# Optimization experiments

Hardware: AMD Instinct MI355X
Metric: run time of the kernel (lower is better)

Reference implementation:

```python
import jax, jax.numpy as jnp
import numpy as np

B, N, NC, DIM, H, D, M, TOPK = 1, 2048, 2048, 1024, 16, 64, 16, 64


def _l2norm(t):
    # F.normalize(t, p=2, dim=-1)
    return t / jnp.clip(jnp.linalg.norm(t, axis=-1, keepdims=True), 1e-12)


def _attn_layer(x, ctx, q_mask, k_mask, Wq, Wk, Wv, th_pre, th_post,
                mem_k, mem_v, scale_p, hs, Wo):
    b, n, _ = x.shape
    h, m, d = mem_k.shape
    nc = ctx.shape[1]
    q = (x @ Wq).reshape(b, n, h, d).transpose(0, 2, 1, 3)      # b h i d
    k = (ctx @ Wk).reshape(b, nc, h, d).transpose(0, 2, 1, 3)   # b h j d
    v = (ctx @ Wv).reshape(b, nc, h, d).transpose(0, 2, 1, 3)
    # memory key/values prepended
    k = jnp.concatenate([jnp.broadcast_to(mem_k[None], (b, h, m, d)), k], axis=2)
    v = jnp.concatenate([jnp.broadcast_to(mem_v[None], (b, h, m, d)), v], axis=2)
    # input mask (q_mask x k_mask), padded True over mem slots
    im = q_mask[:, None, :, None] & k_mask[:, None, None, :]    # b 1 i j
    im = jnp.pad(im, ((0, 0), (0, 0), (0, 0), (m, 0)), constant_values=True)
    # qk_norm: cosine-sim attention with learned per-head scale
    q = _l2norm(q)
    k = _l2norm(k)
    scale = 1.0 / jnp.clip(jnp.exp(scale_p), 0.01)              # [h]
    dots = jnp.einsum('bhid,bhjd->bhij', q, k) * scale[None, :, None, None]
    dots = jnp.einsum('gh,bhij->bgij', th_pre, dots)            # pre-softmax talking heads (1x1 conv over heads)
    neg = -jnp.finfo(dots.dtype).max
    dots = jnp.where(im, dots, neg)
    # sparse topk: keep only the TOPK largest logits per query
    kth = jax.lax.top_k(dots, TOPK)[0][..., -1:]
    dots = jnp.where(dots < kth, neg, dots)
    attn = jax.nn.softmax(dots, axis=-1)
    attn = jnp.einsum('gh,bhij->bgij', th_post, attn)           # post-softmax talking heads
    out = jnp.einsum('bhij,bhjd->bhid', attn, v)
    out = out * hs[None, :, None, None]                          # head scale
    out = out.transpose(0, 2, 1, 3).reshape(b, n, h * d)
    return out @ Wo


def setup_inputs():
    key = jax.random.key(0)
    ks = jax.random.split(key, 18)
    s = 1.0 / np.sqrt(DIM)
    sh = 1.0 / np.sqrt(H)

    def w(i, shape, scale=1.0):
        return jax.random.normal(ks[i], shape, dtype=jnp.float32) * scale

    return {
        'x': w(0, (B, N, DIM)),
        'context': w(1, (2, B, NC, DIM)),
        'mask': jnp.ones((B, N), dtype=bool),
        'context_mask': jnp.ones((B, NC), dtype=bool),
        'Wq1': w(2, (DIM, H * D), s), 'Wk1': w(3, (DIM, H * D), s), 'Wv1': w(4, (DIM, H * D), s),
        'Wq2': w(5, (DIM, H * D), s), 'Wk2': w(6, (DIM, H * D), s), 'Wv2': w(7, (DIM, H * D), s),
        'th_pre1': w(8, (H, H), sh), 'th_post1': w(9, (H, H), sh),
        'th_pre2': w(10, (H, H), sh), 'th_post2': w(11, (H, H), sh),
        'mem_k1': w(12, (H, M, D)), 'mem_v1': w(13, (H, M, D)),
        'mem_k2': w(14, (H, M, D)), 'mem_v2': w(15, (H, M, D)),
        'scale1': jnp.full((H,), -3.0, jnp.float32),
        'scale2': jnp.full((H,), -3.0, jnp.float32),
        'head_scale1': jnp.ones((H,), jnp.float32),
        'head_scale2': jnp.ones((H,), jnp.float32),
        'Wo1': w(16, (H * D, DIM), s), 'Wo2': w(17, (H * D, DIM), s),
    }


def reference(x, context, mask, context_mask,
              Wq1, Wk1, Wv1, Wq2, Wk2, Wv2,
              th_pre1, th_post1, th_pre2, th_post2,
              mem_k1, mem_v1, mem_k2, mem_v2,
              scale1, scale2, head_scale1, head_scale2, Wo1, Wo2):
    x = _attn_layer(x, context[0], mask, context_mask, Wq1, Wk1, Wv1,
                    th_pre1, th_post1, mem_k1, mem_v1, scale1, head_scale1, Wo1)
    x = _attn_layer(x, context[1], mask, context_mask, Wq2, Wk2, Wv2,
                    th_pre2, th_post2, mem_k2, mem_v2, scale2, head_scale2, Wo2)
    return x
```

## Files before the change

kernel.cpp:

```cpp
#include <hip/hip_runtime.h>

#define DEVI __device__ __forceinline__

typedef unsigned short u16;
typedef __attribute__((ext_vector_type(8))) _Float16 f16x8;
typedef __attribute__((ext_vector_type(4))) float f32x4;

#define NQ   2048
#define DIMM 1024
#define HD   16
#define MM   16
#define JTOT 2064
#define JPK  2080
#define JPAD 2112
#define KTOP 64
#define EPITCH 2114

DEVI u16 f2h(float x) {
    _Float16 h = (_Float16)x;
    u16 r; __builtin_memcpy(&r, &h, 2); return r;
}
DEVI void fsplit(float x, u16& hi, u16& lo) {
    _Float16 h = (_Float16)x;
    float r = x - (float)h;
    _Float16 l = (_Float16)r;
    __builtin_memcpy(&hi, &h, 2);
    __builtin_memcpy(&lo, &l, 2);
}

__global__ __launch_bounds__(256) void split1_kernel(
    const float* __restrict__ s, u16* __restrict__ hi, u16* __restrict__ lo, int n4)
{
    int gid = blockIdx.x * 256 + threadIdx.x;
    if (gid < n4) {
        float4 v = ((const float4*)s)[gid];
        ushort4 h, l;
        fsplit(v.x, h.x, l.x); fsplit(v.y, h.y, l.y);
        fsplit(v.z, h.z, l.z); fsplit(v.w, h.w, l.w);
        ((ushort4*)hi)[gid] = h;
        ((ushort4*)lo)[gid] = l;
    }
}

struct P8 { const float* w[8]; };

__global__ __launch_bounds__(256) void wtrans_kernel(P8 src, u16* WTh, u16* WTl) {
    __shared__ float T[64][65];
    const float* W = src.w[blockIdx.z];
    size_t off = (size_t)blockIdx.z * DIMM * DIMM;
    int n0 = blockIdx.x * 64, k0 = blockIdx.y * 64;
#pragma unroll
    for (int rep = 0; rep < 16; ++rep) {
        int idx = rep * 256 + threadIdx.x;
        int kk = idx >> 6, nn = idx & 63;
        T[kk][nn] = W[(size_t)(k0 + kk) * DIMM + n0 + nn];
    }
    __syncthreads();
#pragma unroll
    for (int rep = 0; rep < 16; ++rep) {
        int idx = rep * 256 + threadIdx.x;
        int nn = idx >> 6, kk = idx & 63;
        u16 h, l; fsplit(T[kk][nn], h, l);
        WTh[off + (size_t)(n0 + nn) * DIMM + k0 + kk] = h;
        WTl[off + (size_t)(n0 + nn) * DIMM + k0 + kk] = l;
    }
}

template<int OM>
__global__ __launch_bounds__(256) void gemm_nt(
    const u16* __restrict__ A, int lda, long sA,
    const u16* __restrict__ B, int ldb, long sB,
    void* __restrict__ Cv, int ldc, long sC, int K)
{
    __shared__ u16 As[64 * 40];
    __shared__ u16 Bs[64 * 40];
    const int tid = threadIdx.x;
    const int z = blockIdx.z;
    A += (size_t)z * sA; B += (size_t)z * sB;
    const int bm = blockIdx.x * 64, bn = blockIdx.y * 64;
    const int l = tid & 63, w = tid >> 6;
    const int wm = (w >> 1) * 32, wn = (w & 1) * 32;
    const int srow = tid >> 2, skcol = (tid & 3) * 8;
    const u16* Ag = A + (size_t)(bm + srow) * lda + skcol;
    const u16* Bg = B + (size_t)(bn + srow) * ldb + skcol;
    const int lr = l & 15, lk = (l >> 4) * 8;
    f32x4 acc[2][2] = {};
    for (int k0 = 0; k0 < K; k0 += 32) {
        uint4 av = *(const uint4*)(Ag + k0);
        uint4 bv = *(const uint4*)(Bg + k0);
        __syncthreads();
        *(uint4*)&As[srow * 40 + skcol] = av;
        *(uint4*)&Bs[srow * 40 + skcol] = bv;
        __syncthreads();
        f16x8 a0 = *(const f16x8*)&As[(wm + lr) * 40 + lk];
        f16x8 a1 = *(const f16x8*)&As[(wm + 16 + lr) * 40 + lk];
        f16x8 b0 = *(const f16x8*)&Bs[(wn + lr) * 40 + lk];
        f16x8 b1 = *(const f16x8*)&Bs[(wn + 16 + lr) * 40 + lk];
        acc[0][0] = __builtin_amdgcn_mfma_f32_16x16x32_f16(a0, b0, acc[0][0], 0, 0, 0);
        acc[0][1] = __builtin_amdgcn_mfma_f32_16x16x32_f16(a0, b1, acc[0][1], 0, 0, 0);
        acc[1][0] = __builtin_amdgcn_mfma_f32_16x16x32_f16(a1, b0, acc[1][0], 0, 0, 0);
        acc[1][1] = __builtin_amdgcn_mfma_f32_16x16x32_f16(a1, b1, acc[1][1], 0, 0, 0);
    }
    const int crow0 = bm + wm + (l >> 4) * 4;
    const int ccol0 = bn + wn + lr;
#pragma unroll
    for (int mi = 0; mi < 2; ++mi)
#pragma unroll
        for (int ni = 0; ni < 2; ++ni)
#pragma unroll
            for (int r = 0; r < 4; ++r) {
                int row = crow0 + mi * 16 + r;
                int col = ccol0 + ni * 16;
                if (OM == 0) {
                    float* C = (float*)Cv + (size_t)z * sC;
                    C[(size_t)row * ldc + col] = acc[mi][ni][r];
                } else {
                    u16* C = (u16*)Cv + (size_t)z * sC;
                    C[(size_t)row * ldc + col] = f2h(acc[mi][ni][r]);
                }
            }
}

__global__ __launch_bounds__(256) void gemm3_nt(
    const u16* __restrict__ Ah, const u16* __restrict__ Al, int lda,
    const u16* __restrict__ Bh, const u16* __restrict__ Bl, int ldb,
    float* __restrict__ C, int ldc, int K)
{
    __shared__ u16 Ash[64 * 40];
    __shared__ u16 Asl[64 * 40];
    __shared__ u16 Bsh[64 * 40];
    __shared__ u16 Bsl[64 * 40];
    const int tid = threadIdx.x;
    const int bm = blockIdx.x * 64, bn = blockIdx.y * 64;
    const int l = tid & 63, w = tid >> 6;
    const int wm = (w >> 1) * 32, wn = (w & 1) * 32;
    const int srow = tid >> 2, skcol = (tid & 3) * 8;
    const size_t aoff = (size_t)(bm + srow) * lda + skcol;
    const size_t boff = (size_t)(bn + srow) * ldb + skcol;
    const int lr = l & 15, lk = (l >> 4) * 8;
    f32x4 acc[2][2] = {};
    for (int k0 = 0; k0 < K; k0 += 32) {
        uint4 avh = *(const uint4*)(Ah + aoff + k0);
        uint4 avl = *(const uint4*)(Al + aoff + k0);
        uint4 bvh = *(const uint4*)(Bh + boff + k0);
        uint4 bvl = *(const uint4*)(Bl + boff + k0);
        __syncthreads();
        *(uint4*)&Ash[srow * 40 + skcol] = avh;
        *(uint4*)&Asl[srow * 40 + skcol] = avl;
        *(uint4*)&Bsh[srow * 40 + skcol] = bvh;
        *(uint4*)&Bsl[srow * 40 + skcol] = bvl;
        __syncthreads();
        f16x8 a0h = *(const f16x8*)&Ash[(wm + lr) * 40 + lk];
        f16x8 a1h = *(const f16x8*)&Ash[(wm + 16 + lr) * 40 + lk];
        f16x8 a0l = *(const f16x8*)&Asl[(wm + lr) * 40 + lk];
        f16x8 a1l = *(const f16x8*)&Asl[(wm + 16 + lr) * 40 + lk];
        f16x8 b0h = *(const f16x8*)&Bsh[(wn + lr) * 40 + lk];
        f16x8 b1h = *(const f16x8*)&Bsh[(wn + 16 + lr) * 40 + lk];
        f16x8 b0l = *(const f16x8*)&Bsl[(wn + lr) * 40 + lk];
        f16x8 b1l = *(const f16x8*)&Bsl[(wn + 16 + lr) * 40 + lk];
#define MF(acc_, a_, b_) acc_ = __builtin_amdgcn_mfma_f32_16x16x32_f16(a_, b_, acc_, 0, 0, 0)
        MF(acc[0][0], a0h, b0h); MF(acc[0][0], a0h, b0l); MF(acc[0][0], a0l, b0h);
        MF(acc[0][1], a0h, b1h); MF(acc[0][1], a0h, b1l); MF(acc[0][1], a0l, b1h);
        MF(acc[1][0], a1h, b0h); MF(acc[1][0], a1h, b0l); MF(acc[1][0], a1l, b0h);
        MF(acc[1][1], a1h, b1h); MF(acc[1][1], a1h, b1l); MF(acc[1][1], a1l, b1h);
#undef MF
    }
    const int crow0 = bm + wm + (l >> 4) * 4;
    const int ccol0 = bn + wn + lr;
#pragma unroll
    for (int mi = 0; mi < 2; ++mi)
#pragma unroll
        for (int ni = 0; ni < 2; ++ni)
#pragma unroll
            for (int r = 0; r < 4; ++r)
                C[(size_t)(crow0 + mi * 16 + r) * ldc + ccol0 + ni * 16] = acc[mi][ni][r];
}

__global__ __launch_bounds__(256) void normq_kernel(
    const float* __restrict__ Qf, const float* __restrict__ scp,
    u16* __restrict__ qnh, u16* __restrict__ qnl)
{
    int w = threadIdx.x >> 6, l = threadIdx.x & 63;
    int wid = blockIdx.x * 4 + w;
    int h = wid >> 11, i = wid & 2047;
    float x = Qf[(size_t)i * DIMM + h * 64 + l];
    float ss = x * x;
#pragma unroll
    for (int m = 32; m; m >>= 1) ss += __shfl_xor(ss, m);
    float inv = 1.0f / fmaxf(sqrtf(ss), 1e-12f);
    float sc = 1.0f / fmaxf(expf(scp[h]), 0.01f);
    u16 hh, ll; fsplit(x * inv * sc, hh, ll);
    size_t idx = ((size_t)h * NQ + i) * 64 + l;
    qnh[idx] = hh; qnl[idx] = ll;
}

__global__ __launch_bounds__(256) void buildkn_kernel(
    const float* __restrict__ Kf, const float* __restrict__ mem_k,
    u16* __restrict__ knh, u16* __restrict__ knl)
{
    int w = threadIdx.x >> 6, l = threadIdx.x & 63;
    int wid = blockIdx.x * 4 + w;
    int h = wid / JPK, j = wid - h * JPK;
    float x = (j < MM) ? mem_k[((size_t)h * MM + j) * 64 + l]
            : (j < JTOT) ? Kf[(size_t)(j - MM) * DIMM + h * 64 + l] : 0.0f;
    float ss = x * x;
#pragma unroll
    for (int m = 32; m; m >>= 1) ss += __shfl_xor(ss, m);
    float inv = 1.0f / fmaxf(sqrtf(ss), 1e-12f);
    u16 hh, ll; fsplit(x * inv, hh, ll);
    size_t idx = ((size_t)h * JPK + j) * 64 + l;
    knh[idx] = hh; knl[idx] = ll;
}

__global__ __launch_bounds__(256) void buildvvT_kernel(
    const float* __restrict__ Vf, const float* __restrict__ mem_v,
    const float* __restrict__ hsp, u16* __restrict__ vvT)
{
    __shared__ float T[64][65];
    int h = blockIdx.z, j0 = blockIdx.x * 64;
    float hs = hsp[h];
#pragma unroll
    for (int rep = 0; rep < 16; ++rep) {
        int idx = rep * 256 + threadIdx.x;
        int jl = idx >> 6, d = idx & 63;
        int j = j0 + jl;
        float x = (j < MM) ? mem_v[((size_t)h * MM + j) * 64 + d]
                : (j < JTOT) ? Vf[(size_t)(j - MM) * DIMM + h * 64 + d] : 0.0f;
        T[jl][d] = x * hs;
    }
    __syncthreads();
#pragma unroll
    for (int rep = 0; rep < 16; ++rep) {
        int idx = rep * 256 + threadIdx.x;
        int d = idx >> 6, jl = idx & 63;
        vvT[((size_t)h * 64 + d) * JPAD + j0 + jl] = f2h(T[jl][d]);
    }
}

__global__ __launch_bounds__(256) void dots_kernel(
    const u16* __restrict__ qnh, const u16* __restrict__ qnl,
    const u16* __restrict__ knh, const u16* __restrict__ knl,
    const float* __restrict__ th_pre, float* __restrict__ D,
    int q0, int NQC)
{
    __shared__ float red[4][8][256];
    const int tid = threadIdx.x, l = tid & 63, w = tid >> 6;
    const int it = blockIdx.x * 16;
    const int jt = blockIdx.y * 16;
    const int lr = l & 15, lk = (l >> 4) * 8;
    const int qrow = q0 + it + lr;
    const int jrow = jt + lr;
    f32x4 accg[16] = {};
#pragma unroll
    for (int hh = 0; hh < 4; ++hh) {
        const int h = w * 4 + hh;
        size_t qo = (((size_t)h * NQ + qrow) << 6) + lk;
        size_t ko = (((size_t)h * JPK + jrow) << 6) + lk;
        const f16x8* pah = (const f16x8*)(qnh + qo);
        const f16x8* pal = (const f16x8*)(qnl + qo);
        const f16x8* pbh = (const f16x8*)(knh + ko);
        const f16x8* pbl = (const f16x8*)(knl + ko);
        f16x8 a0h = pah[0], a1h = pah[4];
        f16x8 a0l = pal[0], a1l = pal[4];
        f16x8 b0h = pbh[0], b1h = pbh[4];
        f16x8 b0l = pbl[0], b1l = pbl[4];
        f32x4 ah = {};
        ah = __builtin_amdgcn_mfma_f32_16x16x32_f16(a0h, b0h, ah, 0, 0, 0);
        ah = __builtin_amdgcn_mfma_f32_16x16x32_f16(a1h, b1h, ah, 0, 0, 0);
        ah = __builtin_amdgcn_mfma_f32_16x16x32_f16(a0h, b0l, ah, 0, 0, 0);
        ah = __builtin_amdgcn_mfma_f32_16x16x32_f16(a1h, b1l, ah, 0, 0, 0);
        ah = __builtin_amdgcn_mfma_f32_16x16x32_f16(a0l, b0h, ah, 0, 0, 0);
        ah = __builtin_amdgcn_mfma_f32_16x16x32_f16(a1l, b1h, ah, 0, 0, 0);
#pragma unroll
        for (int g = 0; g < 16; ++g)
            accg[g] += th_pre[g * 16 + h] * ah;
    }
    const int orow = it + (l >> 4) * 4;
    const int col = jt + lr;
#pragma unroll
    for (int ph = 0; ph < 2; ++ph) {
        __syncthreads();
#pragma unroll
        for (int g = 0; g < 8; ++g)
            *(f32x4*)&red[w][g][l * 4] = accg[ph * 8 + g];
        __syncthreads();
#pragma unroll
        for (int gq = 0; gq < 2; ++gq) {
            const int gl = w * 2 + gq;
            f32x4 s = *(const f32x4*)&red[0][gl][l * 4];
            s += *(const f32x4*)&red[1][gl][l * 4];
            s += *(const f32x4*)&red[2][gl][l * 4];
            s += *(const f32x4*)&red[3][gl][l * 4];
            const int g = ph * 8 + gl;
#pragma unroll
            for (int r = 0; r < 4; ++r)
                D[((size_t)(orow + r) * 16 + g) * JPAD + col] = s[r];
        }
    }
}

__global__ __launch_bounds__(256) void smix2_kernel(
    const float* __restrict__ D, const float* __restrict__ th_post,
    u16* __restrict__ P)
{
    __shared__ u16 E[16][EPITCH];
    const int tid = threadIdx.x, l = tid & 63, w = tid >> 6;
    const int i = blockIdx.x;
    for (int hh = 0; hh < 4; ++hh) {
        const int h = w * 4 + hh;
        const float* Dr = D + ((size_t)i * 16 + h) * JPAD;
        float v[33]; unsigned ku[33];
#pragma unroll
        for (int s = 0; s < 33; ++s) {
            int j = s * 64 + l;
            float x = (j < JTOT) ? Dr[j] : -3.0e38f;
            v[s] = x;
            unsigned u = __float_as_uint(x);
            ku[s] = (j < JTOT) ? ((u & 0x80000000u) ? ~u : (u | 0x80000000u)) : 0u;
        }
        unsigned t = 0;
        for (int b = 31; b >= 0; --b) {
            unsigned tc = t | (1u << b);
            int c = 0;
#pragma unroll
            for (int s = 0; s < 33; ++s)
                c += (int)__popcll(__ballot(ku[s] >= tc));
            if (c >= KTOP) t = tc;
        }
        float mx = v[0];
#pragma unroll
        for (int s = 1; s < 33; ++s) mx = fmaxf(mx, v[s]);
#pragma unroll
        for (int m = 32; m; m >>= 1) mx = fmaxf(mx, __shfl_xor(mx, m));
        float den = 0.0f;
#pragma unroll
        for (int s = 0; s < 33; ++s) {
            float ev = (ku[s] >= t) ? __expf(v[s] - mx) : 0.0f;
            v[s] = ev; den += ev;
        }
#pragma unroll
        for (int m = 32; m; m >>= 1) den += __shfl_xor(den, m);
        float inv = 1.0f / den;
#pragma unroll
        for (int s = 0; s < 33; ++s)
            E[h][s * 64 + l] = f2h(v[s] * inv);
    }
    __syncthreads();
    const int g = l & 15, hg = l >> 4, hb = (hg & 1) * 8;
    f16x8 afr;
#pragma unroll
    for (int idx = 0; idx < 8; ++idx) {
        int k = hg * 8 + idx;
        afr[idx] = (_Float16)((k < 16) ? th_post[g * 16 + k] : 0.0f);
    }
    for (int t = w; t < 129; t += 4) {
        const int j = t * 16 + g;
        f16x8 bfr;
#pragma unroll
        for (int idx = 0; idx < 8; ++idx) {
            u16 raw = E[hb + idx][j];
            _Float16 hv; __builtin_memcpy(&hv, &raw, 2);
            bfr[idx] = hv;
        }
        f32x4 c = {};
        c = __builtin_amdgcn_mfma_f32_16x16x32_f16(afr, bfr, c, 0, 0, 0);
#pragma unroll
        for (int r = 0; r < 4; ++r) {
            const int gg = hg * 4 + r;
            P[((size_t)i * 16 + gg) * JPAD + j] = f2h(c[r]);
        }
    }
}

extern "C" void kernel_launch(void* const* d_in, const int* in_sizes, int n_in,
                              void* d_out, int out_size, void* d_ws, size_t ws_size,
                              hipStream_t stream)
{
    (void)in_sizes; (void)n_in; (void)out_size;
    const float* x      = (const float*)d_in[0];
    const float* ctx    = (const float*)d_in[1];
    const float* Wq1    = (const float*)d_in[4];
    const float* Wk1    = (const float*)d_in[5];
    const float* Wv1    = (const float*)d_in[6];
    const float* Wq2    = (const float*)d_in[7];
    const float* Wk2    = (const float*)d_in[8];
    const float* Wv2    = (const float*)d_in[9];
    const float* thpre1 = (const float*)d_in[10];
    const float* thpost1= (const float*)d_in[11];
    const float* thpre2 = (const float*)d_in[12];
    const float* thpost2= (const float*)d_in[13];
    const float* memk1  = (const float*)d_in[14];
    const float* memv1  = (const float*)d_in[15];
    const float* memk2  = (const float*)d_in[16];
    const float* memv2  = (const float*)d_in[17];
    const float* sc1    = (const float*)d_in[18];
    const float* sc2    = (const float*)d_in[19];
    const float* hs1    = (const float*)d_in[20];
    const float* hs2    = (const float*)d_in[21];
    const float* Wo1    = (const float*)d_in[22];
    const float* Wo2    = (const float*)d_in[23];

    char* p = (char*)d_ws;
    auto alloc = [&](size_t n) { char* r = p; p += (n + 255) & ~(size_t)255; return r; };
    u16*   xbh   = (u16*)alloc((size_t)NQ * DIMM * 2);
    u16*   xbl   = (u16*)alloc((size_t)NQ * DIMM * 2);
    u16*   cb0h  = (u16*)alloc((size_t)NQ * DIMM * 2);
    u16*   cb0l  = (u16*)alloc((size_t)NQ * DIMM * 2);
    u16*   cb1h  = (u16*)alloc((size_t)NQ * DIMM * 2);
    u16*   cb1l  = (u16*)alloc((size_t)NQ * DIMM * 2);
    u16*   WTh   = (u16*)alloc((size_t)8 * DIMM * DIMM * 2);
    u16*   WTl   = (u16*)alloc((size_t)8 * DIMM * DIMM * 2);
    float* Qf    = (float*)alloc((size_t)NQ * DIMM * 4);
    float* Kf    = (float*)alloc((size_t)NQ * DIMM * 4);
    float* Vf    = (float*)alloc((size_t)NQ * DIMM * 4);
    u16*   qnh   = (u16*)alloc((size_t)16 * NQ * 64 * 2);
    u16*   qnl   = (u16*)alloc((size_t)16 * NQ * 64 * 2);
    u16*   knh   = (u16*)alloc((size_t)16 * JPK * 64 * 2);
    u16*   knl   = (u16*)alloc((size_t)16 * JPK * 64 * 2);
    u16*   vvT   = (u16*)alloc((size_t)16 * 64 * JPAD * 2);
    u16*   attnA = (u16*)alloc((size_t)NQ * DIMM * 2);
    size_t used = (size_t)(p - (char*)d_ws);

    int NQC = 32;
    for (int cand : {512, 256, 128, 64}) {
        if (used + (size_t)16 * cand * JPAD * 6 + 1024 <= ws_size) { NQC = cand; break; }
    }
    float* Dbuf = (float*)alloc((size_t)16 * NQC * JPAD * 4);
    u16*   Pbuf = (u16*)alloc((size_t)16 * NQC * JPAD * 2);

    const int N4 = (NQ * DIMM) / 4;
    split1_kernel<<<2048, 256, 0, stream>>>(x, xbh, xbl, N4);
    split1_kernel<<<2048, 256, 0, stream>>>(ctx, cb0h, cb0l, N4);
    split1_kernel<<<2048, 256, 0, stream>>>(ctx + (size_t)NQ * DIMM, cb1h, cb1l, N4);
    P8 w8{ { Wq1, Wk1, Wv1, Wo1, Wq2, Wk2, Wv2, Wo2 } };
    wtrans_kernel<<<dim3(16, 16, 8), 256, 0, stream>>>(w8, WTh, WTl);

    auto layer = [&](const u16* inh, const u16* inl,
                     const u16* ctxh, const u16* ctxl, int wbase,
                     const float* thpre, const float* thpost,
                     const float* memk, const float* memv,
                     const float* scp, const float* hsp, int li) {
        size_t o_q = (size_t)(wbase + 0) * DIMM * DIMM;
        size_t o_k = (size_t)(wbase + 1) * DIMM * DIMM;
        size_t o_v = (size_t)(wbase + 2) * DIMM * DIMM;
        size_t o_o = (size_t)(wbase + 3) * DIMM * DIMM;
        gemm3_nt<<<dim3(32, 16), 256, 0, stream>>>(inh, inl, DIMM, WTh + o_q, WTl + o_q, DIMM, Qf, DIMM, DIMM);
        gemm3_nt<<<dim3(32, 16), 256, 0, stream>>>(ctxh, ctxl, DIMM, WTh + o_k, WTl + o_k, DIMM, Kf, DIMM, DIMM);
        gemm_nt<0><<<dim3(32, 16, 1), 256, 0, stream>>>(ctxh, DIMM, 0, WTh + o_v, DIMM, 0, Vf, DIMM, 0, DIMM);
        normq_kernel<<<(16 * NQ) / 4, 256, 0, stream>>>(Qf, scp, qnh, qnl);
        buildkn_kernel<<<(16 * JPK) / 4, 256, 0, stream>>>(Kf, memk, knh, knl);
        buildvvT_kernel<<<dim3(33, 1, 16), 256, 0, stream>>>(Vf, memv, hsp, vvT);
        int nch = NQ / NQC;
        for (int c = 0; c < nch; ++c) {
            int q0 = c * NQC;
            dots_kernel<<<dim3(NQC / 16, JTOT / 16), 256, 0, stream>>>(qnh, qnl, knh, knl, thpre, Dbuf, q0, NQC);
            smix2_kernel<<<NQC, 256, 0, stream>>>(Dbuf, thpost, Pbuf);
            gemm_nt<1><<<dim3(NQC / 64, 1, 16), 256, 0, stream>>>(
                Pbuf, 16 * JPAD, (long)JPAD, vvT, JPAD, (long)64 * JPAD,
                attnA + (size_t)q0 * DIMM, DIMM, 64, JPAD);
        }
        if (li == 0) {
            gemm_nt<0><<<dim3(32, 16, 1), 256, 0, stream>>>(attnA, DIMM, 0, WTh + o_o, DIMM, 0, Qf, DIMM, 0, DIMM);
            split1_kernel<<<2048, 256, 0, stream>>>(Qf, xbh, xbl, N4);
        } else {
            gemm_nt<0><<<dim3(32, 16, 1), 256, 0, stream>>>(attnA, DIMM, 0, WTh + o_o, DIMM, 0, d_out, DIMM, 0, DIMM);
        }
    };

    layer(xbh, xbl, cb0h, cb0l, 0, thpre1, thpost1, memk1, memv1, sc1, hs1, 0);
    layer(xbh, xbl, cb1h, cb1l, 4, thpre2, thpost2, memk2, memv2, sc2, hs2, 1);
}
```

Baseline: 1.647 ms.

## Split fused top-k softmax and head-mix kernel into two kernels

Replaces the fused smix2 kernel, which computed the top-k threshold and softmax for 16 heads into LDS and then mixed heads, with two kernels. The first handles one row per wave across many more blocks and writes the fp16 probabilities to a global buffer. The second applies the post-softmax head mix from global memory across a 2D grid. This drops the large LDS footprint that limited occupancy and raises parallelism, but adds a global round trip for the probabilities, an extra launch per chunk, and a larger workspace that may shrink the query chunk size.

```diff
diff --git a/kernel.cpp b/kernel.cpp
--- a/kernel.cpp
+++ b/kernel.cpp
@@ -14,7 +14,6 @@
 #define JPK  2080
 #define JPAD 2112
 #define KTOP 64
-#define EPITCH 2114
 
 DEVI u16 f2h(float x) {
     _Float16 h = (_Float16)x;
@@ -299,53 +298,56 @@
     }
 }
 
-__global__ __launch_bounds__(256) void smix2_kernel(
-    const float* __restrict__ D, const float* __restrict__ th_post,
+__global__ __launch_bounds__(256) void estats_kernel(
+    const float* __restrict__ D, u16* __restrict__ E)
+{
+    const int w = threadIdx.x >> 6, l = threadIdx.x & 63;
+    const int r = blockIdx.x * 4 + w;
+    const float* Dr = D + (size_t)r * JPAD;
+    float v[33]; unsigned ku[33];
+#pragma unroll
+    for (int s = 0; s < 33; ++s) {
+        int j = s * 64 + l;
+        float x = (j < JTOT) ? Dr[j] : -3.0e38f;
+        v[s] = x;
+        unsigned u = __float_as_uint(x);
+        ku[s] = (j < JTOT) ? ((u & 0x80000000u) ? ~u : (u | 0x80000000u)) : 0u;
+    }
+    unsigned t = 0;
+    for (int b = 31; b >= 0; --b) {
+        unsigned tc = t | (1u << b);
+        int c = 0;
+#pragma unroll
+        for (int s = 0; s < 33; ++s)
+            c += (int)__popcll(__ballot(ku[s] >= tc));
+        if (c >= KTOP) t = tc;
+    }
+    float mx = v[0];
+#pragma unroll
+    for (int s = 1; s < 33; ++s) mx = fmaxf(mx, v[s]);
+#pragma unroll
+    for (int m = 32; m; m >>= 1) mx = fmaxf(mx, __shfl_xor(mx, m));
+    float den = 0.0f;
+#pragma unroll
+    for (int s = 0; s < 33; ++s) {
+        float ev = (ku[s] >= t) ? __expf(v[s] - mx) : 0.0f;
+        v[s] = ev; den += ev;
+    }
+#pragma unroll
+    for (int m = 32; m; m >>= 1) den += __shfl_xor(den, m);
+    float inv = 1.0f / den;
+    u16* Er = E + (size_t)r * JPAD;
+#pragma unroll
+    for (int s = 0; s < 33; ++s)
+        Er[s * 64 + l] = f2h(v[s] * inv);
+}
+
+__global__ __launch_bounds__(256) void mixp_kernel(
+    const u16* __restrict__ E, const float* __restrict__ th_post,
     u16* __restrict__ P)
 {
-    __shared__ u16 E[16][EPITCH];
     const int tid = threadIdx.x, l = tid & 63, w = tid >> 6;
-    const int i = blockIdx.x;
-    for (int hh = 0; hh < 4; ++hh) {
-        const int h = w * 4 + hh;
-        const float* Dr = D + ((size_t)i * 16 + h) * JPAD;
-        float v[33]; unsigned ku[33];
-#pragma unroll
-        for (int s = 0; s < 33; ++s) {
-            int j = s * 64 + l;
-            float x = (j < JTOT) ? Dr[j] : -3.0e38f;
-            v[s] = x;
-            unsigned u = __float_as_uint(x);
-            ku[s] = (j < JTOT) ? ((u & 0x80000000u) ? ~u : (u | 0x80000000u)) : 0u;
-        }
-        unsigned t = 0;
-        for (int b = 31; b >= 0; --b) {
-            unsigned tc = t | (1u << b);
-            int c = 0;
-#pragma unroll
-            for (int s = 0; s < 33; ++s)
-                c += (int)__popcll(__ballot(ku[s] >= tc));
-            if (c >= KTOP) t = tc;
-        }
-        float mx = v[0];
-#pragma unroll
-        for (int s = 1; s < 33; ++s) mx = fmaxf(mx, v[s]);
-#pragma unroll
-        for (int m = 32; m; m >>= 1) mx = fmaxf(mx, __shfl_xor(mx, m));
-        float den = 0.0f;
-#pragma unroll
-        for (int s = 0; s < 33; ++s) {
-            float ev = (ku[s] >= t) ? __expf(v[s] - mx) : 0.0f;
-            v[s] = ev; den += ev;
-        }
-#pragma unroll
-        for (int m = 32; m; m >>= 1) den += __shfl_xor(den, m);
-        float inv = 1.0f / den;
-#pragma unroll
-        for (int s = 0; s < 33; ++s)
-            E[h][s * 64 + l] = f2h(v[s] * inv);
-    }
-    __syncthreads();
+    const int i = blockIdx.x, by = blockIdx.y;
     const int g = l & 15, hg = l >> 4, hb = (hg & 1) * 8;
     f16x8 afr;
 #pragma unroll
@@ -353,22 +355,22 @@
         int k = hg * 8 + idx;
         afr[idx] = (_Float16)((k < 16) ? th_post[g * 16 + k] : 0.0f);
     }
-    for (int t = w; t < 129; t += 4) {
+    const u16* Eb = E + (size_t)i * 16 * JPAD;
+    u16* Pb = P + (size_t)i * 16 * JPAD;
+    for (int t = by * 4 + w; t < 129; t += 16) {
         const int j = t * 16 + g;
         f16x8 bfr;
 #pragma unroll
         for (int idx = 0; idx < 8; ++idx) {
-            u16 raw = E[hb + idx][j];
+            u16 raw = Eb[(size_t)(hb + idx) * JPAD + j];
             _Float16 hv; __builtin_memcpy(&hv, &raw, 2);
             bfr[idx] = hv;
         }
         f32x4 c = {};
         c = __builtin_amdgcn_mfma_f32_16x16x32_f16(afr, bfr, c, 0, 0, 0);
 #pragma unroll
-        for (int r = 0; r < 4; ++r) {
-            const int gg = hg * 4 + r;
-            P[((size_t)i * 16 + gg) * JPAD + j] = f2h(c[r]);
-        }
+        for (int r = 0; r < 4; ++r)
+            Pb[(size_t)(hg * 4 + r) * JPAD + j] = f2h(c[r]);
     }
 }
 
@@ -423,9 +425,10 @@
 
     int NQC = 32;
     for (int cand : {512, 256, 128, 64}) {
-        if (used + (size_t)16 * cand * JPAD * 6 + 1024 <= ws_size) { NQC = cand; break; }
+        if (used + (size_t)16 * cand * JPAD * 8 + 1024 <= ws_size) { NQC = cand; break; }
     }
     float* Dbuf = (float*)alloc((size_t)16 * NQC * JPAD * 4);
+    u16*   Ebuf = (u16*)alloc((size_t)16 * NQC * JPAD * 2);
     u16*   Pbuf = (u16*)alloc((size_t)16 * NQC * JPAD * 2);
 
     const int N4 = (NQ * DIMM) / 4;
@@ -454,7 +457,8 @@
         for (int c = 0; c < nch; ++c) {
             int q0 = c * NQC;
             dots_kernel<<<dim3(NQC / 16, JTOT / 16), 256, 0, stream>>>(qnh, qnl, knh, knl, thpre, Dbuf, q0, NQC);
-            smix2_kernel<<<NQC, 256, 0, stream>>>(Dbuf, thpost, Pbuf);
+            estats_kernel<<<(16 * NQC) / 4, 256, 0, stream>>>(Dbuf, Ebuf);
+            mixp_kernel<<<dim3(NQC, 4), 256, 0, stream>>>(Ebuf, thpost, Pbuf);
             gemm_nt<1><<<dim3(NQC / 64, 1, 16), 256, 0, stream>>>(
                 Pbuf, 16 * JPAD, (long)JPAD, vvT, JPAD, (long)64 * JPAD,
                 attnA + (size_t)q0 * DIMM, DIMM, 64, JPAD);
```

Result: faster. 1.574 ms (-4.4%).
